# Kernel optimization log

Measured on AMD Instinct MI355X. Metric: run time of the kernel, lower is better.

## Reference

```python
import jax, jax.numpy as jnp
import numpy as np

LOW, HIGH = 0.1, 0.3
HYST_ITERS = 16  # fixed-point iterations for hysteresis flood-fill

_GAUSS = jnp.array([[1., 2., 1.], [2., 4., 2.], [1., 2., 1.]], jnp.float32) / 16.0
_SOBEL_X = jnp.array([[-1., 0., 1.], [-2., 0., 2.], [-1., 0., 1.]], jnp.float32)
_SOBEL_Y = jnp.array([[-1., -2., -1.], [0., 0., 0.], [1., 2., 1.]], jnp.float32)


def _conv3x3(x, k):
    # x: [B,H,W,1], k: [3,3] -> SAME conv, stride 1
    return jax.lax.conv_general_dilated(
        x, k.reshape(3, 3, 1, 1), (1, 1), 'SAME',
        dimension_numbers=('NHWC', 'HWIO', 'NHWC'))


def _shift(x, dh, dw):
    # result[b,i,j,c] = x[b,i+dh,j+dw,c], zeros outside the image
    p = jnp.pad(x, ((0, 0), (1, 1), (1, 1), (0, 0)))
    return jax.lax.dynamic_slice(p, (0, 1 + dh, 1 + dw, 0), x.shape)


def setup_inputs() -> dict:
    key = jax.random.key(0)
    inputs = jax.random.uniform(key, (8, 1024, 1024, 1), dtype=jnp.float32)
    return {"inputs": inputs}


def reference(inputs) -> jnp.ndarray:
    # 1) Gaussian blur + Sobel gradients
    blurred = _conv3x3(inputs, _GAUSS)
    gx = _conv3x3(blurred, _SOBEL_X)
    gy = _conv3x3(blurred, _SOBEL_Y)
    mag = jnp.sqrt(gx * gx + gy * gy)
    direction = jnp.arctan2(gy, gx)

    # 2) Non-maximum suppression keyed on quantized gradient direction
    angle = direction * (180.0 / np.pi)
    angle = jnp.where(angle < 0, angle + 180.0, angle)
    b0 = (angle < 22.5) | (angle >= 157.5)          # horizontal gradient -> left/right
    b1 = (angle >= 22.5) & (angle < 67.5)           # 45 deg diagonal
    b2 = (angle >= 67.5) & (angle < 112.5)          # vertical -> up/down
    # b3 (135 deg) is the fallback branch
    n1 = jnp.where(b0, _shift(mag, 0, 1),
         jnp.where(b1, _shift(mag, -1, 1),
         jnp.where(b2, _shift(mag, -1, 0), _shift(mag, -1, -1))))
    n2 = jnp.where(b0, _shift(mag, 0, -1),
         jnp.where(b1, _shift(mag, 1, -1),
         jnp.where(b2, _shift(mag, 1, 0), _shift(mag, 1, 1))))
    suppressed = jnp.where((mag >= n1) & (mag >= n2), mag, 0.0)

    # 3) Double threshold
    strong = jnp.where(suppressed >= HIGH, 1.0, 0.0)
    weak = jnp.where((suppressed >= LOW) & (suppressed < HIGH), 1.0, 0.0)

    # 4) Hysteresis: propagate strong edges through weak pixels (iterated 3x3 dilation)
    def body(i, edges):
        dil = jax.lax.reduce_window(edges, -jnp.inf, jax.lax.max,
                                    (1, 3, 3, 1), (1, 1, 1, 1), 'SAME')
        return jnp.maximum(edges, weak * (dil > 0).astype(edges.dtype))

    edges = jax.lax.fori_loop(0, HYST_ITERS, body, strong)
    return edges
```

## Files before the change

### kernel.cpp

```cpp
#include <hip/hip_runtime.h>
#include <math.h>
#include <stdint.h>

typedef unsigned long long u64;

#define HH 1024
#define WW 1024
#define NB 8
#define WPR 16

__device__ __forceinline__ float blur_at(const float* p) {
#pragma clang fp contract(off)
    float s = p[0] * 0.0625f;
    s += p[1] * 0.125f;
    s += p[2] * 0.0625f;
    s += p[70] * 0.125f;
    s += p[71] * 0.25f;
    s += p[72] * 0.125f;
    s += p[140] * 0.0625f;
    s += p[141] * 0.125f;
    s += p[142] * 0.0625f;
    return s;
}

__device__ __forceinline__ void sobel_at(const float* p, float& osx, float& osy) {
#pragma clang fp contract(off)
    float x00 = p[0], x01 = p[1], x02 = p[2];
    float x10 = p[68], x12 = p[70];
    float x20 = p[136], x21 = p[137], x22 = p[138];
    float gx = -x00;
    gx += x02;
    gx -= 2.f * x10;
    gx += 2.f * x12;
    gx -= x20;
    gx += x22;
    float gy = -x00;
    gy -= 2.f * x01;
    gy -= x02;
    gy += x20;
    gy += 2.f * x21;
    gy += x22;
    osx = gx;
    osy = gy;
}

__device__ __forceinline__ int bucket_exact(float sy, float sx) {
#pragma clang fp contract(off)
    float ang = (float)atan2((double)sy, (double)sx);
    float deg = ang * 57.29577951308232f;
    if (deg < 0.f) deg += 180.f;
    if (deg < 22.5f || deg >= 157.5f) return 0;
    if (deg < 67.5f) return 1;
    if (deg < 112.5f) return 2;
    return 3;
}

__global__ __launch_bounds__(256) void canny_s1(const float* __restrict__ in,
                                                u64* __restrict__ strongB,
                                                u64* __restrict__ weakB) {
#pragma clang fp contract(off)
    const int bx  = blockIdx.x;
    const int b   = bx >> 8;
    const int rem = bx & 255;
    const int y0  = (rem >> 4) << 6;
    const int x0  = (rem & 15) << 6;
    const float* img = in + (size_t)b * (HH * WW);

    __shared__ float sIn[70 * 70];
    __shared__ float sBl[68 * 68];
    float* sMag = sIn;

    const int tid = threadIdx.x;

    for (int idx = tid; idx < 70 * 70; idx += 256) {
        int r = idx / 70, c = idx - r * 70;
        int gy = y0 - 3 + r, gx = x0 - 3 + c;
        float v = 0.f;
        if ((unsigned)gy < HH && (unsigned)gx < WW) v = img[gy * WW + gx];
        sIn[idx] = v;
    }
    __syncthreads();

    for (int idx = tid; idx < 68 * 68; idx += 256) {
        int r = idx / 68, c = idx - r * 68;
        int gy = y0 - 2 + r, gx = x0 - 2 + c;
        float v = 0.f;
        if ((unsigned)gy < HH && (unsigned)gx < WW) v = blur_at(&sIn[r * 70 + c]);
        sBl[idx] = v;
    }
    __syncthreads();

    for (int idx = tid; idx < 66 * 66; idx += 256) {
        int r = idx / 66, c = idx - r * 66;
        int gy = y0 - 1 + r, gx = x0 - 1 + c;
        float v = 0.f;
        if ((unsigned)gy < HH && (unsigned)gx < WW) {
            float sx, sy;
            sobel_at(&sBl[r * 68 + c], sx, sy);
            float xx = sx * sx;
            float yy = sy * sy;
            v = sqrtf(xx + yy);
        }
        sMag[r * 66 + c] = v;
    }
    __syncthreads();

    const int lane = tid & 63;
    const int wv   = tid >> 6;

    for (int y = wv; y < 64; y += 4) {
        float sx, sy;
        sobel_at(&sBl[(y + 1) * 68 + (lane + 1)], sx, sy);

        const int base = (y + 1) * 66 + (lane + 1);
        float m = sMag[base];

        const float t1 = 0.41421356237309503f;
        const float t2 = 2.414213562373095f;
        float ax = fabsf(sx), ay = fabsf(sy);
        float r1 = t1 * ax, r2 = t2 * ax;
        int bucket;
        bool near1 = fabsf(ay - r1) <= 1e-4f * (ay + r1);
        bool near2 = fabsf(ay - r2) <= 1e-4f * (ay + r2);
        if (near1 | near2) {
            bucket = bucket_exact(sy, sx);
        } else if (ay < r1) {
            bucket = 0;
        } else if (ay < r2) {
            bucket = ((sx > 0.f) == (sy > 0.f)) ? 1 : 3;
        } else {
            bucket = 2;
        }

        float n1, n2;
        if (bucket == 0)      { n1 = sMag[base + 1];      n2 = sMag[base - 1]; }
        else if (bucket == 1) { n1 = sMag[base - 66 + 1]; n2 = sMag[base + 66 - 1]; }
        else if (bucket == 2) { n1 = sMag[base - 66];     n2 = sMag[base + 66]; }
        else                  { n1 = sMag[base - 66 - 1]; n2 = sMag[base + 66 + 1]; }

        bool keep = (m >= n1) && (m >= n2);
        bool st = keep && (m >= 0.3f);
        bool wk = keep && (m >= 0.1f) && (m < 0.3f);

        u64 bs = __ballot(st);
        u64 bw = __ballot(wk);
        if (lane == 0) {
            size_t o = (size_t)(b * HH + y0 + y) * WPR + (x0 >> 6);
            strongB[o] = bs;
            weakB[o]   = bw;
        }
    }
}

__global__ __launch_bounds__(256) void canny_s2(const u64* __restrict__ strongB,
                                                const u64* __restrict__ weakB,
                                                float* __restrict__ out) {
    const int wave = threadIdx.x >> 6;
    const int lane = threadIdx.x & 63;
    const int tile = blockIdx.x * 4 + wave;
    const int b   = tile >> 8;
    const int rem = tile & 255;
    const int y0  = (rem >> 4) << 6;
    const int x0  = (rem & 15) << 6;
    const int w0  = (x0 >> 6) - 1;

    u64 e[2][3], k[2][3];
#pragma unroll
    for (int i = 0; i < 2; ++i) {
        int rr = 2 * lane + i;
        int gy = y0 - 16 + rr;
#pragma unroll
        for (int w = 0; w < 3; ++w) {
            int gw = w0 + w;
            u64 s = 0, kk = 0;
            if (rr < 96 && (unsigned)gy < HH && (unsigned)gw < WPR) {
                size_t o = (size_t)(b * HH + gy) * WPR + gw;
                s  = strongB[o];
                kk = weakB[o];
            }
            e[i][w] = s;
            k[i][w] = kk;
        }
    }

    for (int it = 0; it < 16; ++it) {
        u64 hd[2][3];
#pragma unroll
        for (int i = 0; i < 2; ++i)
#pragma unroll
            for (int w = 0; w < 3; ++w) {
                u64 m = e[i][w];
                u64 l = (w > 0) ? e[i][w - 1] : 0ull;
                u64 r = (w < 2) ? e[i][w + 1] : 0ull;
                hd[i][w] = m | (m << 1) | (m >> 1) | (l >> 63) | (r << 63);
            }
#pragma unroll
        for (int w = 0; w < 3; ++w) {
            u64 up = (u64)__shfl_up((long long)hd[1][w], 1);
            if (lane == 0) up = 0ull;
            u64 dn = (u64)__shfl_down((long long)hd[0][w], 1);
            if (lane == 63) dn = 0ull;
            u64 d0 = up | hd[0][w] | hd[1][w];
            u64 d1 = hd[0][w] | hd[1][w] | dn;
            e[0][w] |= k[0][w] & d0;
            e[1][w] |= k[1][w] & d1;
        }
    }

    if (lane >= 8 && lane < 40) {
#pragma unroll
        for (int i = 0; i < 2; ++i) {
            int gy = y0 - 16 + 2 * lane + i;
            u64 word = e[i][1];
            float* orow = out + (size_t)(b * HH + gy) * WW + x0;
            for (int c = 0; c < 64; c += 4) {
                float4 v;
                v.x = ((word >> c) & 1ull)       ? 1.f : 0.f;
                v.y = ((word >> (c + 1)) & 1ull) ? 1.f : 0.f;
                v.z = ((word >> (c + 2)) & 1ull) ? 1.f : 0.f;
                v.w = ((word >> (c + 3)) & 1ull) ? 1.f : 0.f;
                *reinterpret_cast<float4*>(orow + c) = v;
            }
        }
    }
}

extern "C" void kernel_launch(void* const* d_in, const int* in_sizes, int n_in,
                              void* d_out, int out_size, void* d_ws, size_t ws_size,
                              hipStream_t stream) {
    const float* in = (const float*)d_in[0];
    float* out = (float*)d_out;

    u64* strongB = (u64*)d_ws;
    u64* weakB   = strongB + (size_t)NB * HH * WPR;

    canny_s1<<<dim3(NB * 16 * 16), 256, 0, stream>>>(in, strongB, weakB);
    canny_s2<<<dim3(NB * 16 * 16 / 4), 256, 0, stream>>>(strongB, weakB, out);
}
```

Baseline: 147.4 us.

## Vectorize blur/Sobel stages and register-block non-maximum suppression

The blur and Sobel stages now each produce four adjacent outputs per thread, reading shared memory as float4 from a padded 72-float input stride. The Sobel stage also computes the gradient-direction bucket and stores it as bytes in shared memory, so the NMS loop no longer recomputes the Sobel gradients. NMS now processes four rows per wave iteration, keeping a 6x3 window of magnitudes in registers and batching the ballots and bitmask stores. The aim is fewer LDS instructions and less redundant arithmetic. In exchange, bucket classification, including the double-precision atan2 fallback, now also runs on the halo pixels, and register pressure rises.

```diff
diff --git a/kernel.cpp b/kernel.cpp
--- a/kernel.cpp
+++ b/kernel.cpp
@@ -9,40 +9,7 @@
 #define NB 8
 #define WPR 16
 
-__device__ __forceinline__ float blur_at(const float* p) {
-#pragma clang fp contract(off)
-    float s = p[0] * 0.0625f;
-    s += p[1] * 0.125f;
-    s += p[2] * 0.0625f;
-    s += p[70] * 0.125f;
-    s += p[71] * 0.25f;
-    s += p[72] * 0.125f;
-    s += p[140] * 0.0625f;
-    s += p[141] * 0.125f;
-    s += p[142] * 0.0625f;
-    return s;
-}
-
-__device__ __forceinline__ void sobel_at(const float* p, float& osx, float& osy) {
-#pragma clang fp contract(off)
-    float x00 = p[0], x01 = p[1], x02 = p[2];
-    float x10 = p[68], x12 = p[70];
-    float x20 = p[136], x21 = p[137], x22 = p[138];
-    float gx = -x00;
-    gx += x02;
-    gx -= 2.f * x10;
-    gx += 2.f * x12;
-    gx -= x20;
-    gx += x22;
-    float gy = -x00;
-    gy -= 2.f * x01;
-    gy -= x02;
-    gy += x20;
-    gy += 2.f * x21;
-    gy += x22;
-    osx = gx;
-    osy = gy;
-}
+#define SMEM_BYTES 43152
 
 __device__ __forceinline__ int bucket_exact(float sy, float sx) {
 #pragma clang fp contract(off)
@@ -53,6 +20,20 @@
     if (deg < 67.5f) return 1;
     if (deg < 112.5f) return 2;
     return 3;
+}
+
+__device__ __forceinline__ int bucket_of(float sy, float sx) {
+#pragma clang fp contract(off)
+    const float t1 = 0.41421356237309503f;
+    const float t2 = 2.414213562373095f;
+    float ax = fabsf(sx), ay = fabsf(sy);
+    float r1 = t1 * ax, r2 = t2 * ax;
+    bool near1 = fabsf(ay - r1) <= 1e-4f * (ay + r1);
+    bool near2 = fabsf(ay - r2) <= 1e-4f * (ay + r2);
+    if (near1 | near2) return bucket_exact(sy, sx);
+    if (ay < r1) return 0;
+    if (ay < r2) return ((sx > 0.f) == (sy > 0.f)) ? 1 : 3;
+    return 2;
 }
 
 __global__ __launch_bounds__(256) void canny_s1(const float* __restrict__ in,
@@ -66,9 +47,11 @@
     const int x0  = (rem & 15) << 6;
     const float* img = in + (size_t)b * (HH * WW);
 
-    __shared__ float sIn[70 * 70];
-    __shared__ float sBl[68 * 68];
-    float* sMag = sIn;
+    __shared__ __align__(16) char smem[SMEM_BYTES];
+    float* sInF = (float*)smem;
+    float* sBlF = (float*)(smem + 20160);
+    unsigned char* sBkt = (unsigned char*)(smem + 38656);
+    float* sMagF = sInF;
 
     const int tid = threadIdx.x;
 
@@ -77,77 +60,130 @@
         int gy = y0 - 3 + r, gx = x0 - 3 + c;
         float v = 0.f;
         if ((unsigned)gy < HH && (unsigned)gx < WW) v = img[gy * WW + gx];
-        sIn[idx] = v;
+        sInF[r * 72 + c] = v;
     }
     __syncthreads();
 
-    for (int idx = tid; idx < 68 * 68; idx += 256) {
-        int r = idx / 68, c = idx - r * 68;
-        int gy = y0 - 2 + r, gx = x0 - 2 + c;
-        float v = 0.f;
-        if ((unsigned)gy < HH && (unsigned)gx < WW) v = blur_at(&sIn[r * 70 + c]);
-        sBl[idx] = v;
+    for (int q = tid; q < 68 * 17; q += 256) {
+        int r = q / 17, c4 = (q - r * 17) * 4;
+        const float4* p0 = (const float4*)&sInF[r * 72 + c4];
+        const float4* p1 = (const float4*)&sInF[(r + 1) * 72 + c4];
+        const float4* p2 = (const float4*)&sInF[(r + 2) * 72 + c4];
+        float4 a0 = p0[0], b0 = p0[1];
+        float4 a1 = p1[0], b1 = p1[1];
+        float4 a2 = p2[0], b2 = p2[1];
+        float w0[6] = {a0.x, a0.y, a0.z, a0.w, b0.x, b0.y};
+        float w1[6] = {a1.x, a1.y, a1.z, a1.w, b1.x, b1.y};
+        float w2[6] = {a2.x, a2.y, a2.z, a2.w, b2.x, b2.y};
+        int gy = y0 - 2 + r;
+        float4 outv;
+        float res[4];
+#pragma unroll
+        for (int j = 0; j < 4; ++j) {
+            float s = w0[j] * 0.0625f;
+            s += w0[j + 1] * 0.125f;
+            s += w0[j + 2] * 0.0625f;
+            s += w1[j] * 0.125f;
+            s += w1[j + 1] * 0.25f;
+            s += w1[j + 2] * 0.125f;
+            s += w2[j] * 0.0625f;
+            s += w2[j + 1] * 0.125f;
+            s += w2[j + 2] * 0.0625f;
+            int gx = x0 - 2 + c4 + j;
+            res[j] = ((unsigned)gy < HH && (unsigned)gx < WW) ? s : 0.f;
+        }
+        outv.x = res[0]; outv.y = res[1]; outv.z = res[2]; outv.w = res[3];
+        *(float4*)&sBlF[r * 68 + c4] = outv;
     }
     __syncthreads();
 
-    for (int idx = tid; idx < 66 * 66; idx += 256) {
-        int r = idx / 66, c = idx - r * 66;
-        int gy = y0 - 1 + r, gx = x0 - 1 + c;
-        float v = 0.f;
-        if ((unsigned)gy < HH && (unsigned)gx < WW) {
-            float sx, sy;
-            sobel_at(&sBl[r * 68 + c], sx, sy);
-            float xx = sx * sx;
-            float yy = sy * sy;
-            v = sqrtf(xx + yy);
-        }
-        sMag[r * 66 + c] = v;
+    for (int q = tid; q < 66 * 17; q += 256) {
+        int r = q / 17, c4 = (q - r * 17) * 4;
+        const float4* p0 = (const float4*)&sBlF[r * 68 + c4];
+        const float4* p1 = (const float4*)&sBlF[(r + 1) * 68 + c4];
+        const float4* p2 = (const float4*)&sBlF[(r + 2) * 68 + c4];
+        float4 a0 = p0[0], b0 = p0[1];
+        float4 a1 = p1[0], b1 = p1[1];
+        float4 a2 = p2[0], b2 = p2[1];
+        float w0[6] = {a0.x, a0.y, a0.z, a0.w, b0.x, b0.y};
+        float w1[6] = {a1.x, a1.y, a1.z, a1.w, b1.x, b1.y};
+        float w2[6] = {a2.x, a2.y, a2.z, a2.w, b2.x, b2.y};
+        int gy = y0 - 1 + r;
+        float res[4];
+        unsigned bpack = 0;
+#pragma unroll
+        for (int j = 0; j < 4; ++j) {
+            float gxv = -w0[j];
+            gxv += w0[j + 2];
+            gxv -= 2.f * w1[j];
+            gxv += 2.f * w1[j + 2];
+            gxv -= w2[j];
+            gxv += w2[j + 2];
+            float gyv = -w0[j];
+            gyv -= 2.f * w0[j + 1];
+            gyv -= w0[j + 2];
+            gyv += w2[j];
+            gyv += 2.f * w2[j + 1];
+            gyv += w2[j + 2];
+            float xx = gxv * gxv;
+            float yy = gyv * gyv;
+            float v = sqrtf(xx + yy);
+            int gx = x0 - 1 + c4 + j;
+            bool inb = ((unsigned)gy < HH && (unsigned)gx < WW);
+            res[j] = inb ? v : 0.f;
+            int bk = bucket_of(gyv, gxv);
+            bpack |= (unsigned)bk << (8 * j);
+        }
+        float4 outv;
+        outv.x = res[0]; outv.y = res[1]; outv.z = res[2]; outv.w = res[3];
+        *(float4*)&sMagF[r * 68 + c4] = outv;
+        *(unsigned*)&sBkt[r * 68 + c4] = bpack;
     }
     __syncthreads();
 
     const int lane = tid & 63;
     const int wv   = tid >> 6;
-
-    for (int y = wv; y < 64; y += 4) {
-        float sx, sy;
-        sobel_at(&sBl[(y + 1) * 68 + (lane + 1)], sx, sy);
-
-        const int base = (y + 1) * 66 + (lane + 1);
-        float m = sMag[base];
-
-        const float t1 = 0.41421356237309503f;
-        const float t2 = 2.414213562373095f;
-        float ax = fabsf(sx), ay = fabsf(sy);
-        float r1 = t1 * ax, r2 = t2 * ax;
-        int bucket;
-        bool near1 = fabsf(ay - r1) <= 1e-4f * (ay + r1);
-        bool near2 = fabsf(ay - r2) <= 1e-4f * (ay + r2);
-        if (near1 | near2) {
-            bucket = bucket_exact(sy, sx);
-        } else if (ay < r1) {
-            bucket = 0;
-        } else if (ay < r2) {
-            bucket = ((sx > 0.f) == (sy > 0.f)) ? 1 : 3;
-        } else {
-            bucket = 2;
-        }
-
-        float n1, n2;
-        if (bucket == 0)      { n1 = sMag[base + 1];      n2 = sMag[base - 1]; }
-        else if (bucket == 1) { n1 = sMag[base - 66 + 1]; n2 = sMag[base + 66 - 1]; }
-        else if (bucket == 2) { n1 = sMag[base - 66];     n2 = sMag[base + 66]; }
-        else                  { n1 = sMag[base - 66 - 1]; n2 = sMag[base + 66 + 1]; }
-
-        bool keep = (m >= n1) && (m >= n2);
-        bool st = keep && (m >= 0.3f);
-        bool wk = keep && (m >= 0.1f) && (m < 0.3f);
-
-        u64 bs = __ballot(st);
-        u64 bw = __ballot(wk);
+    const int x    = lane;
+
+#pragma unroll
+    for (int s = 0; s < 4; ++s) {
+        int ys = wv * 16 + s * 4;
+        float mm[6][3];
+#pragma unroll
+        for (int rr = 0; rr < 6; ++rr)
+#pragma unroll
+            for (int cc = 0; cc < 3; ++cc)
+                mm[rr][cc] = sMagF[(ys + rr) * 68 + (x + cc)];
+
+        bool st[4], wk[4];
+#pragma unroll
+        for (int j = 0; j < 4; ++j) {
+            int bk = sBkt[(ys + 1 + j) * 68 + (x + 1)];
+            float m = mm[j + 1][1];
+            float n1, n2;
+            if (bk == 0)      { n1 = mm[j + 1][2]; n2 = mm[j + 1][0]; }
+            else if (bk == 1) { n1 = mm[j][2];     n2 = mm[j + 2][0]; }
+            else if (bk == 2) { n1 = mm[j][1];     n2 = mm[j + 2][1]; }
+            else              { n1 = mm[j][0];     n2 = mm[j + 2][2]; }
+            bool keep = (m >= n1) && (m >= n2);
+            st[j] = keep && (m >= 0.3f);
+            wk[j] = keep && (m >= 0.1f) && (m < 0.3f);
+        }
+
+        u64 bs0 = __ballot(st[0]), bs1 = __ballot(st[1]);
+        u64 bs2 = __ballot(st[2]), bs3 = __ballot(st[3]);
+        u64 bw0 = __ballot(wk[0]), bw1 = __ballot(wk[1]);
+        u64 bw2 = __ballot(wk[2]), bw3 = __ballot(wk[3]);
         if (lane == 0) {
-            size_t o = (size_t)(b * HH + y0 + y) * WPR + (x0 >> 6);
-            strongB[o] = bs;
-            weakB[o]   = bw;
+            size_t o = (size_t)(b * HH + y0 + ys) * WPR + (x0 >> 6);
+            strongB[o]           = bs0;
+            strongB[o + WPR]     = bs1;
+            strongB[o + 2 * WPR] = bs2;
+            strongB[o + 3 * WPR] = bs3;
+            weakB[o]             = bw0;
+            weakB[o + WPR]       = bw1;
+            weakB[o + 2 * WPR]   = bw2;
+            weakB[o + 3 * WPR]   = bw3;
         }
     }
 }
@@ -200,10 +236,8 @@
             if (lane == 0) up = 0ull;
             u64 dn = (u64)__shfl_down((long long)hd[0][w], 1);
             if (lane == 63) dn = 0ull;
-            u64 d0 = up | hd[0][w] | hd[1][w];
-            u64 d1 = hd[0][w] | hd[1][w] | dn;
-            e[0][w] |= k[0][w] & d0;
-            e[1][w] |= k[1][w] & d1;
+            e[0][w] |= k[0][w] & (up | hd[0][w] | hd[1][w]);
+            e[1][w] |= k[1][w] & (hd[0][w] | hd[1][w] | dn);
         }
     }
 
```

After: 149.6 us. Within noise of the previous version (+1.5%).
